# Performance work log

Hardware: AMD Instinct MI355X
Metric: run time of the kernel (lower is better)

The kernel has to match this reference:

```python
import jax, jax.numpy as jnp
import numpy as np

B, T, H = 32, 2048, 512
D = 2 * H  # bidirectional encoder feature dim


def setup_inputs() -> dict:
    key = jax.random.key(0)
    k1, k2, k3, k4, k5 = jax.random.split(key, 5)
    stdv = 1.0 / np.sqrt(H)
    return {
        "hidden": jax.random.normal(k1, (B, D), dtype=jnp.float32),
        "encoder_outputs": jax.random.normal(k2, (B, T, D), dtype=jnp.float32),
        "W_attn": jax.random.normal(k3, (H, 2 * D), dtype=jnp.float32) * stdv,
        "b_attn": jax.random.normal(k4, (H,), dtype=jnp.float32) * stdv,
        "v": jax.random.normal(k5, (H,), dtype=jnp.float32) * stdv,
    }


def reference(hidden, encoder_outputs, W_attn, b_attn, v):
    # The original per-timestep sliding-window loop recomputes a position-wise
    # Linear+tanh+dot whose value is independent of the window index, and
    # overlapping writes overwrite with identical values. The exact same math
    # is full additive attention over all T positions.
    d = encoder_outputs.shape[-1]
    Wh = W_attn[:, :d]   # acts on repeated decoder hidden state
    We = W_attn[:, d:]   # acts on encoder outputs
    # [B, H] ; avoids materializing the [B, T, 4H] concat
    hid_proj = jnp.einsum('bd,hd->bh', hidden, Wh)
    # [B, T, H]
    energy = jnp.tanh(jnp.einsum('btd,hd->bth', encoder_outputs, We)
                      + hid_proj[:, None, :] + b_attn)
    scores = jnp.einsum('bth,h->bt', energy, v)  # [B, T]
    return jax.nn.softmax(scores, axis=1)[:, None, :]  # [B, 1, T]
```

## Files before the change

### kernel.cpp

```cpp
#include <hip/hip_runtime.h>

#define Bv 32
#define Tv 2048
#define Hv 512
#define Dv 1024

using bf16x8 = __attribute__((ext_vector_type(8))) __bf16;
using bf16x4 = __attribute__((ext_vector_type(4))) __bf16;
using f32x4  = __attribute__((ext_vector_type(4))) float;

__global__ void prep_kernel(const float* __restrict__ hidden,
                            const float* __restrict__ W,
                            const float* __restrict__ b_attn,
                            bf16x8* __restrict__ We_sw,
                            float* __restrict__ hp) {
    int h   = blockIdx.x;
    int tid = threadIdx.x;

    if (tid < 128) {
        int d = tid * 8;
        const float* src = W + h * (2 * Dv) + Dv + d;
        float4 f0 = *(const float4*)src;
        float4 f1 = *(const float4*)(src + 4);
        bf16x8 o;
        o[0] = (__bf16)f0.x; o[1] = (__bf16)f0.y; o[2] = (__bf16)f0.z; o[3] = (__bf16)f0.w;
        o[4] = (__bf16)f1.x; o[5] = (__bf16)f1.y; o[6] = (__bf16)f1.z; o[7] = (__bf16)f1.w;
        int s = ((h >> 4) * 32 + (d >> 5)) * 64 + (((d >> 3) & 3) << 4) + (h & 15);
        We_sw[s] = o;
    }

    float4 wh = ((const float4*)(W + h * (2 * Dv)))[tid];
    __shared__ float red[4][Bv];
    int lane = tid & 63, w = tid >> 6;
    for (int b = 0; b < Bv; ++b) {
        float4 x = ((const float4*)(hidden + b * Dv))[tid];
        float p = wh.x * x.x + wh.y * x.y + wh.z * x.z + wh.w * x.w;
#pragma unroll
        for (int m = 1; m < 64; m <<= 1) p += __shfl_xor(p, m);
        if (lane == 0) red[w][b] = p;
    }
    __syncthreads();
    if (tid < Bv)
        hp[tid * Hv + h] = red[0][tid] + red[1][tid] + red[2][tid] + red[3][tid] + b_attn[h];
}

__device__ __forceinline__ float fast_tanh(float x) {
    float xc = fminf(fmaxf(x, -9.0f), 9.0f);
    float e  = __expf(2.0f * xc);
    return 1.0f - 2.0f / (e + 1.0f);
}

__global__ __launch_bounds__(512, 4) void attn_main(
    const float* __restrict__ enc, const bf16x8* __restrict__ Bg,
    const float* __restrict__ hp, const float* __restrict__ vvec,
    float* __restrict__ scores)
{
    __shared__ __align__(16) __bf16 Abuf[2][64 * 72];
    __shared__ float redbuf[8][64];

    const int tid   = threadIdx.x;
    const int lane  = tid & 63;
    const int w     = tid >> 6;
    const int row0  = blockIdx.x * 64;
    const int batch = row0 >> 11;

    const int srow = tid >> 3;
    const int sd0  = (tid & 7) * 4;
    const float* gA = enc + (row0 + srow) * Dv + sd0;
    __bf16* lw0 = &Abuf[0][srow * 72 + sd0];

    const bf16x8* Bptr = Bg + (w * 4 * 32) * 64 + lane;

    f32x4 acc[4][4];
#pragma unroll
    for (int i = 0; i < 4; ++i)
#pragma unroll
        for (int j = 0; j < 4; ++j)
            acc[i][j] = (f32x4){0.f, 0.f, 0.f, 0.f};

    float4 f0 = *(const float4*)gA;
    float4 f1 = *(const float4*)(gA + 32);

    const int arow  = lane & 15;
    const int acol8 = (lane >> 4) * 8;

    for (int kc = 0; kc < 16; ++kc) {
        __bf16* p = lw0 + (kc & 1) * (64 * 72);
        bf16x4 o0, o1;
        o0[0] = (__bf16)f0.x; o0[1] = (__bf16)f0.y; o0[2] = (__bf16)f0.z; o0[3] = (__bf16)f0.w;
        o1[0] = (__bf16)f1.x; o1[1] = (__bf16)f1.y; o1[2] = (__bf16)f1.z; o1[3] = (__bf16)f1.w;
        *(bf16x4*)p        = o0;
        *(bf16x4*)(p + 32) = o1;
        if (kc < 15) {
            f0 = *(const float4*)(gA + (kc + 1) * 64);
            f1 = *(const float4*)(gA + (kc + 1) * 64 + 32);
        }
        bf16x8 Bc[2][4];
#pragma unroll
        for (int ktl = 0; ktl < 2; ++ktl)
#pragma unroll
            for (int j = 0; j < 4; ++j)
                Bc[ktl][j] = Bptr[(j * 32 + kc * 2 + ktl) * 64];

        __builtin_amdgcn_sched_barrier(0);
        asm volatile("s_waitcnt lgkmcnt(0)" ::: "memory");
        __builtin_amdgcn_s_barrier();
        __builtin_amdgcn_sched_barrier(0);

        const __bf16* rb = &Abuf[kc & 1][0];
#pragma unroll
        for (int ktl = 0; ktl < 2; ++ktl) {
            bf16x8 a0 = *(const bf16x8*)(rb + (0 * 16 + arow) * 72 + ktl * 32 + acol8);
            bf16x8 a1 = *(const bf16x8*)(rb + (1 * 16 + arow) * 72 + ktl * 32 + acol8);
            bf16x8 a2 = *(const bf16x8*)(rb + (2 * 16 + arow) * 72 + ktl * 32 + acol8);
            bf16x8 a3 = *(const bf16x8*)(rb + (3 * 16 + arow) * 72 + ktl * 32 + acol8);
            __builtin_amdgcn_s_setprio(1);
#pragma unroll
            for (int j = 0; j < 4; ++j) {
                acc[0][j] = __builtin_amdgcn_mfma_f32_16x16x32_bf16(a0, Bc[ktl][j], acc[0][j], 0, 0, 0);
                acc[1][j] = __builtin_amdgcn_mfma_f32_16x16x32_bf16(a1, Bc[ktl][j], acc[1][j], 0, 0, 0);
                acc[2][j] = __builtin_amdgcn_mfma_f32_16x16x32_bf16(a2, Bc[ktl][j], acc[2][j], 0, 0, 0);
                acc[3][j] = __builtin_amdgcn_mfma_f32_16x16x32_bf16(a3, Bc[ktl][j], acc[3][j], 0, 0, 0);
            }
            __builtin_amdgcn_s_setprio(0);
        }
    }

    float hpv[4], vv[4];
#pragma unroll
    for (int j = 0; j < 4; ++j) {
        int n  = w * 64 + j * 16 + (lane & 15);
        hpv[j] = hp[batch * Hv + n];
        vv[j]  = vvec[n];
    }
    const int qrow = (lane >> 4) * 4;
#pragma unroll
    for (int mt = 0; mt < 4; ++mt)
#pragma unroll
        for (int r = 0; r < 4; ++r) {
            float p = 0.f;
#pragma unroll
            for (int j = 0; j < 4; ++j)
                p += vv[j] * fast_tanh(acc[mt][j][r] + hpv[j]);
            p += __shfl_xor(p, 1);
            p += __shfl_xor(p, 2);
            p += __shfl_xor(p, 4);
            p += __shfl_xor(p, 8);
            if ((lane & 15) == 0)
                redbuf[w][mt * 16 + qrow + r] = p;
        }
    __syncthreads();
    if (tid < 64) {
        float s = 0.f;
#pragma unroll
        for (int ww = 0; ww < 8; ++ww) s += redbuf[ww][tid];
        scores[row0 + tid] = s;
    }
}

__global__ void softmax_kernel(const float* __restrict__ scores, float* __restrict__ out) {
    int b   = blockIdx.x;
    int tid = threadIdx.x;
    const float* s = scores + b * Tv;
    float local[4];
    float m = -1e30f;
#pragma unroll
    for (int i = 0; i < 4; ++i) { local[i] = s[tid + i * 512]; m = fmaxf(m, local[i]); }
    __shared__ float red[8];
    int lane = tid & 63, w = tid >> 6;
#pragma unroll
    for (int x = 1; x < 64; x <<= 1) m = fmaxf(m, __shfl_xor(m, x));
    if (lane == 0) red[w] = m;
    __syncthreads();
#pragma unroll
    for (int ww = 0; ww < 8; ++ww) m = fmaxf(m, red[ww]);
    float sum = 0.f;
#pragma unroll
    for (int i = 0; i < 4; ++i) { local[i] = __expf(local[i] - m); sum += local[i]; }
#pragma unroll
    for (int x = 1; x < 64; x <<= 1) sum += __shfl_xor(sum, x);
    __syncthreads();
    if (lane == 0) red[w] = sum;
    __syncthreads();
    sum = 0.f;
#pragma unroll
    for (int ww = 0; ww < 8; ++ww) sum += red[ww];
    float inv = 1.0f / sum;
#pragma unroll
    for (int i = 0; i < 4; ++i) out[b * Tv + tid + i * 512] = local[i] * inv;
}

extern "C" void kernel_launch(void* const* d_in, const int* in_sizes, int n_in,
                              void* d_out, int out_size, void* d_ws, size_t ws_size,
                              hipStream_t stream) {
    const float* hidden = (const float*)d_in[0];
    const float* enc    = (const float*)d_in[1];
    const float* W      = (const float*)d_in[2];
    const float* b_attn = (const float*)d_in[3];
    const float* v      = (const float*)d_in[4];
    float* out = (float*)d_out;

    char* ws = (char*)d_ws;
    bf16x8* We_sw = (bf16x8*)ws;
    float*  hp    = (float*)(ws + (1 << 20));
    float*  sc    = (float*)(ws + (1 << 20) + (1 << 16));

    prep_kernel<<<Hv, 256, 0, stream>>>(hidden, W, b_attn, We_sw, hp);
    attn_main<<<(Bv * Tv) / 64, 512, 0, stream>>>(enc, We_sw, hp, v, sc);
    softmax_kernel<<<Bv, 512, 0, stream>>>(sc, out);
}
```

Baseline: 454.9 us.

## Double K-chunk to 128 and prefetch encoder rows two chunks ahead

The main GEMM loop now processes K in 8 chunks of 128 instead of 16 chunks of 64. This halves the number of block barriers. Global loads of encoder rows are issued two chunks ahead, and the LDS stores for the next chunk are interleaved with the MFMAs of the current one. The aim is to hide global load latency and reduce synchronization overhead, at the cost of more registers and LDS per block, which may reduce occupancy.

Result: no change. 452.2 us (-0.6%).

```diff
diff --git a/kernel.cpp b/kernel.cpp
--- a/kernel.cpp
+++ b/kernel.cpp
@@ -55,7 +55,7 @@
     const float* __restrict__ hp, const float* __restrict__ vvec,
     float* __restrict__ scores)
 {
-    __shared__ __align__(16) __bf16 Abuf[2][64 * 72];
+    __shared__ __align__(16) __bf16 Abuf[2][64 * 136];
     __shared__ float redbuf[8][64];
 
     const int tid   = threadIdx.x;
@@ -67,9 +67,11 @@
     const int srow = tid >> 3;
     const int sd0  = (tid & 7) * 4;
     const float* gA = enc + (row0 + srow) * Dv + sd0;
-    __bf16* lw0 = &Abuf[0][srow * 72 + sd0];
 
     const bf16x8* Bptr = Bg + (w * 4 * 32) * 64 + lane;
+
+    const int arow  = lane & 15;
+    const int acol8 = (lane >> 4) * 8;
 
     f32x4 acc[4][4];
 #pragma unroll
@@ -78,53 +80,77 @@
         for (int j = 0; j < 4; ++j)
             acc[i][j] = (f32x4){0.f, 0.f, 0.f, 0.f};
 
-    float4 f0 = *(const float4*)gA;
-    float4 f1 = *(const float4*)(gA + 32);
-
-    const int arow  = lane & 15;
-    const int acol8 = (lane >> 4) * 8;
-
-    for (int kc = 0; kc < 16; ++kc) {
-        __bf16* p = lw0 + (kc & 1) * (64 * 72);
-        bf16x4 o0, o1;
-        o0[0] = (__bf16)f0.x; o0[1] = (__bf16)f0.y; o0[2] = (__bf16)f0.z; o0[3] = (__bf16)f0.w;
-        o1[0] = (__bf16)f1.x; o1[1] = (__bf16)f1.y; o1[2] = (__bf16)f1.z; o1[3] = (__bf16)f1.w;
-        *(bf16x4*)p        = o0;
-        *(bf16x4*)(p + 32) = o1;
-        if (kc < 15) {
-            f0 = *(const float4*)(gA + (kc + 1) * 64);
-            f1 = *(const float4*)(gA + (kc + 1) * 64 + 32);
+    float4 fA[4], fB[4];
+    {
+#pragma unroll
+        for (int s = 0; s < 4; ++s) fA[s] = *(const float4*)(gA + s * 32);
+        __bf16* wb = &Abuf[0][srow * 136 + sd0];
+#pragma unroll
+        for (int s = 0; s < 4; ++s) {
+            bf16x4 o;
+            o[0] = (__bf16)fA[s].x; o[1] = (__bf16)fA[s].y;
+            o[2] = (__bf16)fA[s].z; o[3] = (__bf16)fA[s].w;
+            *(bf16x4*)(wb + s * 32) = o;
         }
-        bf16x8 Bc[2][4];
-#pragma unroll
-        for (int ktl = 0; ktl < 2; ++ktl)
-#pragma unroll
-            for (int j = 0; j < 4; ++j)
-                Bc[ktl][j] = Bptr[(j * 32 + kc * 2 + ktl) * 64];
-
-        __builtin_amdgcn_sched_barrier(0);
-        asm volatile("s_waitcnt lgkmcnt(0)" ::: "memory");
-        __builtin_amdgcn_s_barrier();
-        __builtin_amdgcn_sched_barrier(0);
-
-        const __bf16* rb = &Abuf[kc & 1][0];
-#pragma unroll
-        for (int ktl = 0; ktl < 2; ++ktl) {
-            bf16x8 a0 = *(const bf16x8*)(rb + (0 * 16 + arow) * 72 + ktl * 32 + acol8);
-            bf16x8 a1 = *(const bf16x8*)(rb + (1 * 16 + arow) * 72 + ktl * 32 + acol8);
-            bf16x8 a2 = *(const bf16x8*)(rb + (2 * 16 + arow) * 72 + ktl * 32 + acol8);
-            bf16x8 a3 = *(const bf16x8*)(rb + (3 * 16 + arow) * 72 + ktl * 32 + acol8);
-            __builtin_amdgcn_s_setprio(1);
-#pragma unroll
-            for (int j = 0; j < 4; ++j) {
-                acc[0][j] = __builtin_amdgcn_mfma_f32_16x16x32_bf16(a0, Bc[ktl][j], acc[0][j], 0, 0, 0);
-                acc[1][j] = __builtin_amdgcn_mfma_f32_16x16x32_bf16(a1, Bc[ktl][j], acc[1][j], 0, 0, 0);
-                acc[2][j] = __builtin_amdgcn_mfma_f32_16x16x32_bf16(a2, Bc[ktl][j], acc[2][j], 0, 0, 0);
-                acc[3][j] = __builtin_amdgcn_mfma_f32_16x16x32_bf16(a3, Bc[ktl][j], acc[3][j], 0, 0, 0);
-            }
-            __builtin_amdgcn_s_setprio(0);
-        }
-    }
+#pragma unroll
+        for (int s = 0; s < 4; ++s) fB[s] = *(const float4*)(gA + 128 + s * 32);
+    }
+
+#define CHUNK_BODY(K, FW, FL)                                                   \
+    {                                                                           \
+        __builtin_amdgcn_sched_barrier(0);                                      \
+        asm volatile("s_waitcnt lgkmcnt(0)" ::: "memory");                      \
+        __builtin_amdgcn_s_barrier();                                           \
+        __builtin_amdgcn_sched_barrier(0);                                      \
+        const __bf16* rb = &Abuf[(K) & 1][0];                                   \
+        __bf16* wb = &Abuf[((K) + 1) & 1][srow * 136 + sd0];                    \
+        _Pragma("unroll")                                                       \
+        for (int s = 0; s < 4; ++s) {                                           \
+            bf16x8 Bc0 = Bptr[(0 * 32 + (K) * 4 + s) * 64];                     \
+            bf16x8 Bc1 = Bptr[(1 * 32 + (K) * 4 + s) * 64];                     \
+            bf16x8 Bc2 = Bptr[(2 * 32 + (K) * 4 + s) * 64];                     \
+            bf16x8 Bc3 = Bptr[(3 * 32 + (K) * 4 + s) * 64];                     \
+            if ((K) <= 5) FL[s] = *(const float4*)(gA + ((K) + 2) * 128 + s * 32); \
+            bf16x8 a0 = *(const bf16x8*)(rb + (0 * 16 + arow) * 136 + s * 32 + acol8); \
+            bf16x8 a1 = *(const bf16x8*)(rb + (1 * 16 + arow) * 136 + s * 32 + acol8); \
+            bf16x8 a2 = *(const bf16x8*)(rb + (2 * 16 + arow) * 136 + s * 32 + acol8); \
+            bf16x8 a3 = *(const bf16x8*)(rb + (3 * 16 + arow) * 136 + s * 32 + acol8); \
+            __builtin_amdgcn_s_setprio(1);                                      \
+            acc[0][0] = __builtin_amdgcn_mfma_f32_16x16x32_bf16(a0, Bc0, acc[0][0], 0, 0, 0); \
+            acc[1][0] = __builtin_amdgcn_mfma_f32_16x16x32_bf16(a1, Bc0, acc[1][0], 0, 0, 0); \
+            acc[2][0] = __builtin_amdgcn_mfma_f32_16x16x32_bf16(a2, Bc0, acc[2][0], 0, 0, 0); \
+            acc[3][0] = __builtin_amdgcn_mfma_f32_16x16x32_bf16(a3, Bc0, acc[3][0], 0, 0, 0); \
+            acc[0][1] = __builtin_amdgcn_mfma_f32_16x16x32_bf16(a0, Bc1, acc[0][1], 0, 0, 0); \
+            acc[1][1] = __builtin_amdgcn_mfma_f32_16x16x32_bf16(a1, Bc1, acc[1][1], 0, 0, 0); \
+            acc[2][1] = __builtin_amdgcn_mfma_f32_16x16x32_bf16(a2, Bc1, acc[2][1], 0, 0, 0); \
+            acc[3][1] = __builtin_amdgcn_mfma_f32_16x16x32_bf16(a3, Bc1, acc[3][1], 0, 0, 0); \
+            acc[0][2] = __builtin_amdgcn_mfma_f32_16x16x32_bf16(a0, Bc2, acc[0][2], 0, 0, 0); \
+            acc[1][2] = __builtin_amdgcn_mfma_f32_16x16x32_bf16(a1, Bc2, acc[1][2], 0, 0, 0); \
+            acc[2][2] = __builtin_amdgcn_mfma_f32_16x16x32_bf16(a2, Bc2, acc[2][2], 0, 0, 0); \
+            acc[3][2] = __builtin_amdgcn_mfma_f32_16x16x32_bf16(a3, Bc2, acc[3][2], 0, 0, 0); \
+            acc[0][3] = __builtin_amdgcn_mfma_f32_16x16x32_bf16(a0, Bc3, acc[0][3], 0, 0, 0); \
+            acc[1][3] = __builtin_amdgcn_mfma_f32_16x16x32_bf16(a1, Bc3, acc[1][3], 0, 0, 0); \
+            acc[2][3] = __builtin_amdgcn_mfma_f32_16x16x32_bf16(a2, Bc3, acc[2][3], 0, 0, 0); \
+            acc[3][3] = __builtin_amdgcn_mfma_f32_16x16x32_bf16(a3, Bc3, acc[3][3], 0, 0, 0); \
+            __builtin_amdgcn_s_setprio(0);                                      \
+            if ((K) <= 6) {                                                     \
+                bf16x4 o;                                                       \
+                o[0] = (__bf16)FW[s].x; o[1] = (__bf16)FW[s].y;                 \
+                o[2] = (__bf16)FW[s].z; o[3] = (__bf16)FW[s].w;                 \
+                *(bf16x4*)(wb + s * 32) = o;                                    \
+            }                                                                   \
+        }                                                                       \
+    }
+
+    CHUNK_BODY(0, fB, fA)
+    CHUNK_BODY(1, fA, fB)
+    CHUNK_BODY(2, fB, fA)
+    CHUNK_BODY(3, fA, fB)
+    CHUNK_BODY(4, fB, fA)
+    CHUNK_BODY(5, fA, fB)
+    CHUNK_BODY(6, fB, fA)
+    CHUNK_BODY(7, fA, fB)
+#undef CHUNK_BODY
 
     float hpv[4], vv[4];
 #pragma unroll
```
